# Kernel optimization log

Hardware: AMD Instinct MI355X
Metric: run time of the kernel (lower is better)

## Reference

```python
import jax, jax.numpy as jnp
import numpy as np

N_EXPERTS = 48
D_IN = 2 * 1280 * 8 * 8  # 163840
D_OUT = 2


def setup_inputs() -> dict:
    key = jax.random.key(0)
    k_x, k_t, k_w, k_b = jax.random.split(key, 4)
    B = 512
    x = jax.random.normal(k_x, (B, 2, 1280, 8, 8), dtype=jnp.float32)
    t = jax.random.randint(k_t, (B,), 0, N_EXPERTS)  # torch code uses t[i]-1; neg index wraps
    # nn.Linear default init: U(-1/sqrt(fan_in), 1/sqrt(fan_in))
    bound = 1.0 / np.sqrt(D_IN)
    W = jax.random.uniform(k_w, (N_EXPERTS, D_IN, D_OUT), dtype=jnp.float32,
                           minval=-bound, maxval=bound)
    b = jax.random.uniform(k_b, (N_EXPERTS, D_OUT), dtype=jnp.float32,
                           minval=-bound, maxval=bound)
    return {"x": x, "t": t, "W": W, "b": b}


def reference(x, t, W, b):
    # x: [B, 2, 1280, 8, 8] -> [B, D_IN]; per-sample expert indexed by t-1
    B = x.shape[0]
    xf = x.reshape(B, -1)  # [B, D_IN]
    idx = (t - 1) % N_EXPERTS  # matches torch negative indexing for t=0
    Wg = W[idx]  # [B, D_IN, D_OUT]
    bg = b[idx]  # [B, D_OUT]
    out = jnp.einsum('bd,bdk->bk', xf, Wg) + bg  # [B, D_OUT]
    return out
```

## Files before the change

kernel.cpp:

```cpp
#include <hip/hip_runtime.h>

#define N_EXPERTS 48
#define D_IN 163840
#define D_OUT 2
#define BATCH 512
#define SPLIT 8
#define CHUNK (D_IN / SPLIT)
#define THREADS 256
#define ITERS (CHUNK / 4 / THREADS)

typedef float nfloat4 __attribute__((ext_vector_type(4)));

__global__ __launch_bounds__(BATCH) void bucket_kernel(const int* __restrict__ t,
                                                       int* __restrict__ ws) {
    __shared__ int cnt[N_EXPERTS];
    __shared__ int off[N_EXPERTS];
    const int s = threadIdx.x;
    if (s < N_EXPERTS) cnt[s] = 0;
    __syncthreads();
    const int e = (t[s] + N_EXPERTS - 1) % N_EXPERTS;
    const int rank = atomicAdd(&cnt[e], 1);
    __syncthreads();
    if (s == 0) {
        int acc = 0;
        for (int i = 0; i < N_EXPERTS; ++i) { off[i] = acc; acc += cnt[i]; }
    }
    __syncthreads();
    const int slot = off[e] + rank;
    ws[slot] = s;
    ws[BATCH + slot] = e;
}

__global__ void init_out_kernel(const int* __restrict__ t,
                                const float* __restrict__ b,
                                float* __restrict__ out) {
    int i = blockIdx.x * blockDim.x + threadIdx.x;
    if (i < BATCH * D_OUT) {
        int s = i >> 1;
        int k = i & 1;
        int e = (t[s] + N_EXPERTS - 1) % N_EXPERTS;
        out[i] = b[e * D_OUT + k];
    }
}

__global__ __launch_bounds__(THREADS) void moe_dot_kernel(
        const float* __restrict__ x,
        const int* __restrict__ ws,
        const float* __restrict__ W,
        float* __restrict__ out) {
    const int chunk = blockIdx.x;
    const int slot  = blockIdx.y;
    const int sample = ws[slot];
    const int e      = ws[BATCH + slot];

    const nfloat4* __restrict__ xp =
        (const nfloat4*)(x + (size_t)sample * D_IN + (size_t)chunk * CHUNK);
    const float4* __restrict__ wp =
        (const float4*)(W + (size_t)e * D_IN * D_OUT + (size_t)chunk * CHUNK * D_OUT);

    float acc0 = 0.f, acc1 = 0.f;

#pragma unroll 4
    for (int it = 0; it < ITERS; ++it) {
        const int i = it * THREADS + threadIdx.x;
        nfloat4 xv = __builtin_nontemporal_load(&xp[i]);
        float4 w0 = wp[2 * i];
        float4 w1 = wp[2 * i + 1];
        acc0 += xv.x * w0.x + xv.y * w0.z + xv.z * w1.x + xv.w * w1.z;
        acc1 += xv.x * w0.y + xv.y * w0.w + xv.z * w1.y + xv.w * w1.w;
    }

    for (int off = 32; off > 0; off >>= 1) {
        acc0 += __shfl_down(acc0, off);
        acc1 += __shfl_down(acc1, off);
    }

    __shared__ float s0[THREADS / 64];
    __shared__ float s1[THREADS / 64];
    const int wid  = threadIdx.x >> 6;
    const int lane = threadIdx.x & 63;
    if (lane == 0) { s0[wid] = acc0; s1[wid] = acc1; }
    __syncthreads();

    if (threadIdx.x == 0) {
        float a0 = s0[0] + s0[1] + s0[2] + s0[3];
        float a1 = s1[0] + s1[1] + s1[2] + s1[3];
        atomicAdd(&out[sample * D_OUT + 0], a0);
        atomicAdd(&out[sample * D_OUT + 1], a1);
    }
}

extern "C" void kernel_launch(void* const* d_in, const int* in_sizes, int n_in,
                              void* d_out, int out_size, void* d_ws, size_t ws_size,
                              hipStream_t stream) {
    const float* x = (const float*)d_in[0];
    const int*   t = (const int*)d_in[1];
    const float* W = (const float*)d_in[2];
    const float* b = (const float*)d_in[3];
    float* out = (float*)d_out;
    int* ws = (int*)d_ws;

    bucket_kernel<<<1, BATCH, 0, stream>>>(t, ws);

    init_out_kernel<<<(BATCH * D_OUT + THREADS - 1) / THREADS, THREADS, 0, stream>>>(
        t, b, out);

    dim3 grid(SPLIT, BATCH);
    moe_dot_kernel<<<grid, THREADS, 0, stream>>>(x, ws, W, out);
}
```

Before: 480.8 us.

## Regroup MoE dot by expert so weight chunks stay in registers across samples

The grid now spans (chunk, expert) instead of (chunk, sample). Each block loads its expert's weight chunk into registers once, then loops over every sample routed to that expert, streaming x and reducing per wavefront with atomics. This cuts repeated weight reads across samples that share an expert. In exchange, per-block work varies with expert occupancy and there are more atomics, one per wavefront per sample per chunk.

```diff
diff --git a/kernel.cpp b/kernel.cpp
--- a/kernel.cpp
+++ b/kernel.cpp
@@ -4,17 +4,17 @@
 #define D_IN 163840
 #define D_OUT 2
 #define BATCH 512
-#define SPLIT 8
-#define CHUNK (D_IN / SPLIT)
+#define CHUNK_E 4096
+#define NCHUNK (D_IN / CHUNK_E)
 #define THREADS 256
-#define ITERS (CHUNK / 4 / THREADS)
+#define F4T (CHUNK_E / 4 / THREADS)
 
 typedef float nfloat4 __attribute__((ext_vector_type(4)));
 
 __global__ __launch_bounds__(BATCH) void bucket_kernel(const int* __restrict__ t,
                                                        int* __restrict__ ws) {
     __shared__ int cnt[N_EXPERTS];
-    __shared__ int off[N_EXPERTS];
+    __shared__ int off[N_EXPERTS + 1];
     const int s = threadIdx.x;
     if (s < N_EXPERTS) cnt[s] = 0;
     __syncthreads();
@@ -24,11 +24,11 @@
     if (s == 0) {
         int acc = 0;
         for (int i = 0; i < N_EXPERTS; ++i) { off[i] = acc; acc += cnt[i]; }
+        off[N_EXPERTS] = acc;
     }
     __syncthreads();
-    const int slot = off[e] + rank;
-    ws[slot] = s;
-    ws[BATCH + slot] = e;
+    ws[off[e] + rank] = s;
+    if (s <= N_EXPERTS) ws[BATCH + s] = off[s];
 }
 
 __global__ void init_out_kernel(const int* __restrict__ t,
@@ -49,44 +49,48 @@
         const float* __restrict__ W,
         float* __restrict__ out) {
     const int chunk = blockIdx.x;
-    const int slot  = blockIdx.y;
-    const int sample = ws[slot];
-    const int e      = ws[BATCH + slot];
+    const int e     = blockIdx.y;
+    const int start = ws[BATCH + e];
+    const int end   = ws[BATCH + e + 1];
+    if (start == end) return;
 
-    const nfloat4* __restrict__ xp =
-        (const nfloat4*)(x + (size_t)sample * D_IN + (size_t)chunk * CHUNK);
-    const float4* __restrict__ wp =
-        (const float4*)(W + (size_t)e * D_IN * D_OUT + (size_t)chunk * CHUNK * D_OUT);
+    const int tid = threadIdx.x;
 
-    float acc0 = 0.f, acc1 = 0.f;
-
-#pragma unroll 4
-    for (int it = 0; it < ITERS; ++it) {
-        const int i = it * THREADS + threadIdx.x;
-        nfloat4 xv = __builtin_nontemporal_load(&xp[i]);
-        float4 w0 = wp[2 * i];
-        float4 w1 = wp[2 * i + 1];
-        acc0 += xv.x * w0.x + xv.y * w0.z + xv.z * w1.x + xv.w * w1.z;
-        acc1 += xv.x * w0.y + xv.y * w0.w + xv.z * w1.y + xv.w * w1.w;
+    const float4* __restrict__ wq =
+        (const float4*)(W + (size_t)e * D_IN * D_OUT + (size_t)chunk * CHUNK_E * D_OUT);
+    float4 w[2 * F4T];
+#pragma unroll
+    for (int j = 0; j < F4T; ++j) {
+        const int i = tid + THREADS * j;
+        w[2 * j]     = wq[2 * i];
+        w[2 * j + 1] = wq[2 * i + 1];
     }
 
-    for (int off = 32; off > 0; off >>= 1) {
-        acc0 += __shfl_down(acc0, off);
-        acc1 += __shfl_down(acc1, off);
-    }
+    const int lane = tid & 63;
 
-    __shared__ float s0[THREADS / 64];
-    __shared__ float s1[THREADS / 64];
-    const int wid  = threadIdx.x >> 6;
-    const int lane = threadIdx.x & 63;
-    if (lane == 0) { s0[wid] = acc0; s1[wid] = acc1; }
-    __syncthreads();
+    for (int slot = start; slot < end; ++slot) {
+        const int sample = ws[slot];
+        const nfloat4* __restrict__ xp =
+            (const nfloat4*)(x + (size_t)sample * D_IN + (size_t)chunk * CHUNK_E);
 
-    if (threadIdx.x == 0) {
-        float a0 = s0[0] + s0[1] + s0[2] + s0[3];
-        float a1 = s1[0] + s1[1] + s1[2] + s1[3];
-        atomicAdd(&out[sample * D_OUT + 0], a0);
-        atomicAdd(&out[sample * D_OUT + 1], a1);
+        float acc0 = 0.f, acc1 = 0.f;
+#pragma unroll
+        for (int j = 0; j < F4T; ++j) {
+            nfloat4 xv = __builtin_nontemporal_load(&xp[tid + THREADS * j]);
+            float4 w0 = w[2 * j];
+            float4 w1 = w[2 * j + 1];
+            acc0 += xv.x * w0.x + xv.y * w0.z + xv.z * w1.x + xv.w * w1.z;
+            acc1 += xv.x * w0.y + xv.y * w0.w + xv.z * w1.y + xv.w * w1.w;
+        }
+
+        for (int off = 32; off > 0; off >>= 1) {
+            acc0 += __shfl_down(acc0, off);
+            acc1 += __shfl_down(acc1, off);
+        }
+        if (lane == 0) {
+            atomicAdd(&out[sample * D_OUT + 0], acc0);
+            atomicAdd(&out[sample * D_OUT + 1], acc1);
+        }
     }
 }
 
@@ -105,6 +109,6 @@
     init_out_kernel<<<(BATCH * D_OUT + THREADS - 1) / THREADS, THREADS, 0, stream>>>(
         t, b, out);
 
-    dim3 grid(SPLIT, BATCH);
+    dim3 grid(NCHUNK, N_EXPERTS);
     moe_dot_kernel<<<grid, THREADS, 0, stream>>>(x, ws, W, out);
 }
```

After: 512.1 us. +6.5%, slower.
